# Kernel optimization log

Measured on AMD Instinct MI355X. Metric: run time of the kernel, lower is better.

Reference implementation:

```python
import jax, jax.numpy as jnp
import numpy as np
import math

IN_F, OUT_F, GRID = 1024, 1024, 7
BATCH, SEQ = 4, 4096


def _l2norm(v, eps=1e-12):
    return v / (jnp.linalg.norm(v) + eps)


def setup_inputs() -> dict:
    key = jax.random.key(0)
    k0, k1, k2, k3 = jax.random.split(key, 4)
    x = jax.random.normal(k0, (BATCH, SEQ, IN_F), dtype=jnp.float32)
    # spectral-normed base linear (weights nonzero for a meaningful baseline)
    base_w = jax.random.normal(k1, (OUT_F, IN_F), dtype=jnp.float32) * 0.02
    base_b = jnp.zeros((OUT_F,), dtype=jnp.float32)
    u = jax.random.normal(k2, (OUT_F,), dtype=jnp.float32)  # power-iteration buffer
    # Chebyshev translation points and fixed logspace scales (as in __init__)
    steps = jnp.arange(GRID, dtype=jnp.float32)
    translation = (-jnp.cos((2.0 * steps + 1.0) / (2.0 * GRID) * math.pi) * 1.5).reshape(1, 1, GRID)
    scale = (1.0 * jnp.logspace(-0.5, 0.5, GRID)).reshape(1, 1, GRID).astype(jnp.float32)
    wavelet_w = jax.random.normal(k3, (OUT_F, IN_F * GRID), dtype=jnp.float32) * 0.01
    soft_threshold = jnp.array([0.005], dtype=jnp.float32)
    output_scale = jnp.array([1.0], dtype=jnp.float32)
    return dict(x=x, base_w=base_w, base_b=base_b, u=u, translation=translation,
                scale=scale, wavelet_w=wavelet_w, soft_threshold=soft_threshold,
                output_scale=output_scale)


def reference(x, base_w, base_b, u, translation, scale, wavelet_w, soft_threshold, output_scale):
    x_flat = x.reshape(-1, x.shape[-1])  # [N, IN]
    # spectral norm: one power iteration (no grad through u, v), sigma = u' W v
    v = jax.lax.stop_gradient(_l2norm(base_w.T @ u))
    u2 = jax.lax.stop_gradient(_l2norm(base_w @ v))
    sigma = u2 @ (base_w @ v)
    w_sn = base_w / sigma
    base_out = jax.nn.silu(x_flat) @ w_sn.T + base_b  # [N, OUT]
    # wavelet (Ricker) basis expansion
    safe_scale = jnp.maximum(jnp.abs(scale), 0.1)  # [1,1,G]
    x_norm = jnp.tanh(x_flat) * 2.5  # [N, IN]
    xe = (x_norm[:, :, None] - translation) / safe_scale  # [N, IN, G]
    basis = (1.0 - xe * xe) * jnp.exp(-0.5 * xe * xe)
    kan = basis.reshape(x_flat.shape[0], -1) @ wavelet_w.T  # [N, OUT]
    thr = jax.nn.softplus(soft_threshold)
    kan = jnp.sign(kan) * jax.nn.relu(jnp.abs(kan) - thr)
    out = (base_out + kan) * output_scale
    return out.reshape(*x.shape[:-1], wavelet_w.shape[0])
```

## Files before the change

kernel.cpp:

```cpp
#include <hip/hip_runtime.h>
#include <math.h>


typedef __attribute__((ext_vector_type(4))) float  f32x4;
typedef __attribute__((ext_vector_type(8))) __bf16 bf16x8;
typedef __attribute__((ext_vector_type(8))) unsigned short u16x8;

#define NROWS 16384
#define INF   1024
#define OUTF  1024
#define GG    7
#define KKAN  7168
#define KTOT  8192

static __device__ __forceinline__ unsigned short f2bf(float f) {
  union { float f; unsigned int u; } v; v.f = f;
  unsigned int r = v.u + 0x7fffu + ((v.u >> 16) & 1u);
  return (unsigned short)(r >> 16);
}

__global__ void mv_wt_u(const float* __restrict__ W, const float* __restrict__ u,
                        float* __restrict__ t) {
  int j = blockIdx.x;
  int tid = threadIdx.x;
  float p = 0.f;
  for (int i = tid; i < OUTF; i += 256) p += W[(size_t)i * INF + j] * u[i];
  __shared__ float red[256];
  red[tid] = p; __syncthreads();
  for (int s = 128; s > 0; s >>= 1) { if (tid < s) red[tid] += red[tid + s]; __syncthreads(); }
  if (tid == 0) t[j] = red[0];
}

__global__ void mv_w_t(const float* __restrict__ W, const float* __restrict__ t,
                       float* __restrict__ s) {
  int i = blockIdx.x;
  int tid = threadIdx.x;
  float p = 0.f;
  for (int j = tid; j < INF; j += 256) p += W[(size_t)i * INF + j] * t[j];
  __shared__ float red[256];
  red[tid] = p; __syncthreads();
  for (int k = 128; k > 0; k >>= 1) { if (tid < k) red[tid] += red[tid + k]; __syncthreads(); }
  if (tid == 0) s[i] = red[0];
}

__global__ void sigma_finish(const float* __restrict__ t, const float* __restrict__ s,
                             const float* __restrict__ st, const float* __restrict__ os,
                             float* __restrict__ scal) {
  __shared__ float r1[256], r2[256];
  int tid = threadIdx.x;
  float p1 = 0.f, p2 = 0.f;
  for (int i = tid; i < 1024; i += 256) { float a = t[i]; p1 += a * a; float b = s[i]; p2 += b * b; }
  r1[tid] = p1; r2[tid] = p2; __syncthreads();
  for (int k = 128; k > 0; k >>= 1) { if (tid < k) { r1[tid] += r1[tid + k]; r2[tid] += r2[tid + k]; } __syncthreads(); }
  if (tid == 0) {
    float nt = sqrtf(r1[0]);
    float ns = sqrtf(r2[0]);
    float nq = ns / (nt + 1e-12f);
    float sigma = nq * nq / (nq + 1e-12f);
    scal[0] = 1.f / sigma;
    scal[1] = log1pf(__expf(st[0]));
    scal[2] = os[0];
  }
}

__global__ void wsn_cast(const float* __restrict__ w, const float* __restrict__ scal,
                         unsigned short* __restrict__ Wp) {
  float is = scal[0];
  int idx = blockIdx.x * 256 + threadIdx.x;
  int row = idx >> 7, i0 = (idx & 127) << 3;
  const f32x4* p = (const f32x4*)(w + (size_t)row * INF + i0);
  f32x4 a = p[0], b = p[1];
  u16x8 v;
  v[0] = f2bf(a[0] * is); v[1] = f2bf(a[1] * is); v[2] = f2bf(a[2] * is); v[3] = f2bf(a[3] * is);
  v[4] = f2bf(b[0] * is); v[5] = f2bf(b[1] * is); v[6] = f2bf(b[2] * is); v[7] = f2bf(b[3] * is);
  *(u16x8*)(Wp + (size_t)row * KTOT + KKAN + i0) = v;
}

__global__ void wkan_cast(const float* __restrict__ w, unsigned short* __restrict__ Wp) {
  __shared__ float row[KKAN];
  int orow = blockIdx.x;
  const float* src = w + (size_t)orow * KKAN;
  for (int c = threadIdx.x * 4; c < KKAN; c += 1024)
    *(f32x4*)&row[c] = *(const f32x4*)&src[c];
  __syncthreads();
  unsigned short* dst = Wp + (size_t)orow * KTOT;
  for (int r = threadIdx.x; r < 896; r += 256) {
    int g = r >> 7, i0 = (r & 127) << 3;
    u16x8 v;
#pragma unroll
    for (int j = 0; j < 8; j++) v[j] = f2bf(row[(i0 + j) * GG + g]);
    *(u16x8*)(dst + g * 1024 + i0) = v;
  }
}

__global__ void expand_kernel(const float* __restrict__ x,
                              const float* __restrict__ translation,
                              const float* __restrict__ scale,
                              unsigned short* __restrict__ Ap,
                              int row0, int nrows) {
  float tr[GG], iss[GG];
#pragma unroll
  for (int g = 0; g < GG; g++) {
    tr[g] = translation[g];
    float s = fabsf(scale[g]);
    iss[g] = 1.f / (s < 0.1f ? 0.1f : s);
  }
  int units = nrows * (INF / 8);
  int stride = gridDim.x * blockDim.x;
  for (int uu = blockIdx.x * blockDim.x + threadIdx.x; uu < units; uu += stride) {
    int nloc = uu >> 7;
    int i0 = (uu & 127) << 3;
    const f32x4* xp = (const f32x4*)(x + (size_t)(row0 + nloc) * INF + i0);
    f32x4 xa = xp[0], xb = xp[1];
    float xv[8] = {xa[0], xa[1], xa[2], xa[3], xb[0], xb[1], xb[2], xb[3]};
    u16x8 sb, kb[GG];
#pragma unroll
    for (int j = 0; j < 8; j++) {
      float xx = xv[j];
      float si = xx / (1.f + __expf(-xx));
      sb[j] = f2bf(si);
      float e2 = __expf(2.f * xx);
      float xn = 2.5f * (1.f - 2.f / (e2 + 1.f));
#pragma unroll
      for (int g = 0; g < GG; g++) {
        float xe = (xn - tr[g]) * iss[g];
        float t2 = xe * xe;
        float b = (1.f - t2) * __expf(-0.5f * t2);
        kb[g][j] = f2bf(b);
      }
    }
    unsigned short* rp = Ap + (size_t)nloc * KTOT;
    *(u16x8*)(rp + KKAN + i0) = sb;
#pragma unroll
    for (int g = 0; g < GG; g++) *(u16x8*)(rp + g * 1024 + i0) = kb[g];
  }
}

static __device__ __forceinline__ void gload16(const unsigned short* g, unsigned short* l) {
  __builtin_amdgcn_global_load_lds(
      (const __attribute__((address_space(1))) unsigned int*)g,
      (__attribute__((address_space(3))) unsigned int*)l, 16, 0, 0);
}

#define SCB   __builtin_amdgcn_sched_barrier(0)
#define SBAR  do { SCB; __builtin_amdgcn_s_barrier(); } while (0)
#define VM(N) asm volatile("s_waitcnt vmcnt(" #N ")" ::: "memory")
#define LG(N) asm volatile("s_waitcnt lgkmcnt(" #N ")" ::: "memory")

#define STAGE(db, tt) do { \
    const unsigned short* _sa = gA + (size_t)(tt) * 64; \
    const unsigned short* _sb = gB + (size_t)(tt) * 64; \
    unsigned short* _da = ldsS + (db) * 24576; \
    unsigned short* _db = ldsS + (db) * 24576 + 16384; \
    gload16(_sa,                       _da); \
    gload16(_sa + (size_t)64  * KTOT,  _da + 4096); \
    gload16(_sa + (size_t)128 * KTOT,  _da + 8192); \
    gload16(_sa + (size_t)192 * KTOT,  _da + 12288); \
    gload16(_sb,                       _db); \
    gload16(_sb + (size_t)64  * KTOT,  _db + 4096); \
  } while (0)

#define RD_A(dst, bb, kx) do { _Pragma("unroll") for (int i = 0; i < 4; ++i) \
    dst[i] = *(const bf16x8*)(pA + (bb) * 49152 + i * 2048 + (kx)); } while (0)

#define RD_B(dst, bb, kx) do { _Pragma("unroll") for (int j = 0; j < 4; ++j) \
    dst[j] = *(const bf16x8*)(pB + (bb) * 49152 + j * 2048 + (kx)); } while (0)

#define MM16(AF, BF) do { _Pragma("unroll") for (int i = 0; i < 4; ++i) \
    _Pragma("unroll") for (int j = 0; j < 4; ++j) \
      acc[i][j] = __builtin_amdgcn_mfma_f32_16x16x32_bf16(AF[i], BF[j], acc[i][j], 0, 0, 0); } while (0)

#define TILE(tt, bb, db, SS, WAIT) do { \
    RD_A(af0, bb, kx0); RD_B(bf0r, bb, kx0); \
    SCB; \
    RD_A(af1, bb, kx1); RD_B(bf1r, bb, kx1); \
    SCB; \
    if (SS) STAGE(db, (tt) + 2); \
    SCB; \
    LG(8); SCB; \
    __builtin_amdgcn_s_setprio(1); MM16(af0, bf0r); __builtin_amdgcn_s_setprio(0); \
    LG(0); SCB; \
    __builtin_amdgcn_s_setprio(1); MM16(af1, bf1r); __builtin_amdgcn_s_setprio(0); \
    WAIT; \
    SBAR; \
  } while (0)

__global__ __launch_bounds__(512, 2) void gemm_k(
    const unsigned short* __restrict__ A,
    const unsigned short* __restrict__ W,
    const float* __restrict__ bias,
    const float* __restrict__ scal,
    float* __restrict__ out) {
  __shared__ unsigned short lds[73728];

  int bid = blockIdx.x;
  int cpx = gridDim.x >> 3;
  int swz = (bid & 7) * cpx + (bid >> 3);
  int m0 = (swz >> 3) * 256;
  int n0 = (swz & 7) * 128;
  int tid = threadIdx.x;
  int wv = tid >> 6, l = tid & 63;
  int wr = wv >> 1, wc = wv & 1;

  float thr = scal[1], osc = scal[2];

  int rowq = tid >> 3;
  int swk = ((tid & 7) ^ (rowq & 7)) << 3;
  const unsigned short* gA = A + (size_t)(m0 + rowq) * KTOT + swk;
  const unsigned short* gB = W + (size_t)(n0 + rowq) * KTOT + swk;
  unsigned short* ldsS = lds + wv * 512;

  int lr = l & 15;
  int kx0 = (((l >> 4) << 4) ^ ((l & 7) << 4));
  int kx1 = kx0 ^ 64;
  const char* pA = (const char*)lds + (wr * 64 + lr) * 128;
  const char* pB = (const char*)lds + 32768 + (wc * 64 + lr) * 128;

  bf16x8 af0[4], af1[4], bf0r[4], bf1r[4];
  f32x4 acc[4][4] = {};

  STAGE(0, 0);
  STAGE(1, 1);
  VM(6);
  SBAR;

  for (int t = 0; t < 108; t += 3) {
    TILE(t,     0, 2, 1, VM(6));
    TILE(t + 1, 1, 0, 1, VM(6));
    TILE(t + 2, 2, 1, 1, VM(6));
  }
  TILE(108, 0, 2, 1, VM(6));
  TILE(109, 1, 0, 1, VM(6));
  TILE(110, 2, 1, 1, VM(6));
  TILE(111, 0, 2, 1, VM(6));

#pragma unroll
  for (int i = 0; i < 4; ++i)
#pragma unroll
    for (int j = 0; j < 4; ++j)
#pragma unroll
      for (int e = 0; e < 4; ++e) {
        float v = acc[i][j][e];
        float a = fabsf(v) - thr;
        a = a > 0.f ? a : 0.f;
        acc[i][j][e] = v > 0.f ? a : -a;
      }

  for (int t = 112; t < 124; t += 3) {
    TILE(t,     1, 0, 1, VM(6));
    TILE(t + 1, 2, 1, 1, VM(6));
    TILE(t + 2, 0, 2, 1, VM(6));
  }
  TILE(124, 1, 0, 1, VM(6));
  TILE(125, 2, 1, 1, VM(6));
  TILE(126, 0, 2, 0, VM(0));
  TILE(127, 1, 2, 0, (void)0);

  int rr = m0 + wr * 64 + ((l >> 4) << 2);
  int cc = n0 + wc * 64 + lr;
#pragma unroll
  for (int i = 0; i < 4; ++i)
#pragma unroll
    for (int j = 0; j < 4; ++j) {
      int c = cc + j * 16;
      float bc = bias[c];
#pragma unroll
      for (int e = 0; e < 4; ++e) {
        int r = rr + i * 16 + e;
        out[(size_t)r * OUTF + c] = (acc[i][j][e] + bc) * osc;
      }
    }
}

extern "C" void kernel_launch(void* const* d_in, const int* in_sizes, int n_in,
                              void* d_out, int out_size, void* d_ws, size_t ws_size,
                              hipStream_t stream) {
  const float* x              = (const float*)d_in[0];
  const float* base_w         = (const float*)d_in[1];
  const float* base_b         = (const float*)d_in[2];
  const float* u              = (const float*)d_in[3];
  const float* translation    = (const float*)d_in[4];
  const float* scale          = (const float*)d_in[5];
  const float* wavelet_w      = (const float*)d_in[6];
  const float* soft_threshold = (const float*)d_in[7];
  const float* output_scale   = (const float*)d_in[8];
  float* out = (float*)d_out;

  char* ws = (char*)d_ws;
  float* t_vec = (float*)ws;
  float* s_vec = t_vec + 1024;
  float* scal  = s_vec + 1024;
  unsigned short* Wp = (unsigned short*)(ws + 16384);
  char* dynbuf = ws + 16384 + (size_t)KTOT * OUTF * 2;

  size_t fixed = 16384 + (size_t)KTOT * OUTF * 2;
  size_t avail = ws_size > fixed ? ws_size - fixed : 0;

  mv_wt_u<<<1024, 256, 0, stream>>>(base_w, u, t_vec);
  mv_w_t<<<1024, 256, 0, stream>>>(base_w, t_vec, s_vec);
  sigma_finish<<<1, 256, 0, stream>>>(t_vec, s_vec, soft_threshold, output_scale, scal);
  wsn_cast<<<512, 256, 0, stream>>>(base_w, scal, Wp);
  wkan_cast<<<1024, 256, 0, stream>>>(wavelet_w, Wp);

  const size_t ROW = (size_t)KTOT * 2;
  size_t total = (size_t)NROWS * ROW;
  int nch = (int)((total + (avail > 0 ? avail : 1) - 1) / (avail > 0 ? avail : 1));
  if (nch < 1) nch = 1;
  long mc = (((NROWS + nch - 1) / nch) + 255) & ~255L;
  while (mc > 256 && (size_t)mc * ROW > avail) mc -= 256;
  if (mc < 256) mc = 256;

  unsigned short* Ap = (unsigned short*)dynbuf;

  for (long r0 = 0; r0 < NROWS; r0 += mc) {
    long nr = (NROWS - r0 < mc) ? (NROWS - r0) : mc;
    expand_kernel<<<2048, 256, 0, stream>>>(x, translation, scale, Ap, (int)r0, (int)nr);
    int mt = (int)(nr / 256);
    gemm_k<<<mt * 8, 512, 0, stream>>>(Ap, Wp, base_b, scal, out + (size_t)r0 * OUTF);
  }
}
```

Baseline: 333.6 us.

## Switch GEMM to 32x32x16 MFMA and coalesce the W^T u matvec

```diff
diff --git a/kernel.cpp b/kernel.cpp
--- a/kernel.cpp
+++ b/kernel.cpp
@@ -2,9 +2,10 @@
 #include <math.h>
 
 
-typedef __attribute__((ext_vector_type(4))) float  f32x4;
-typedef __attribute__((ext_vector_type(8))) __bf16 bf16x8;
-typedef __attribute__((ext_vector_type(8))) unsigned short u16x8;
+typedef __attribute__((ext_vector_type(4)))  float  f32x4;
+typedef __attribute__((ext_vector_type(16))) float  f32x16;
+typedef __attribute__((ext_vector_type(8)))  __bf16 bf16x8;
+typedef __attribute__((ext_vector_type(8)))  unsigned short u16x8;
 
 #define NROWS 16384
 #define INF   1024
@@ -19,16 +20,24 @@
   return (unsigned short)(r >> 16);
 }
 
-__global__ void mv_wt_u(const float* __restrict__ W, const float* __restrict__ u,
+__global__ void zero_t(float* __restrict__ t) { t[threadIdx.x] = 0.f; }
+
+__global__ void wtu_acc(const float* __restrict__ W, const float* __restrict__ u,
                         float* __restrict__ t) {
-  int j = blockIdx.x;
   int tid = threadIdx.x;
-  float p = 0.f;
-  for (int i = tid; i < OUTF; i += 256) p += W[(size_t)i * INF + j] * u[i];
-  __shared__ float red[256];
-  red[tid] = p; __syncthreads();
-  for (int s = 128; s > 0; s >>= 1) { if (tid < s) red[tid] += red[tid + s]; __syncthreads(); }
-  if (tid == 0) t[j] = red[0];
+  int j4 = tid * 4;
+  int i0 = blockIdx.x * 16;
+  f32x4 acc = {0.f, 0.f, 0.f, 0.f};
+  for (int i = i0; i < i0 + 16; ++i) {
+    float ui = u[i];
+    f32x4 w4 = *(const f32x4*)(W + (size_t)i * INF + j4);
+    acc[0] += w4[0] * ui; acc[1] += w4[1] * ui;
+    acc[2] += w4[2] * ui; acc[3] += w4[3] * ui;
+  }
+  atomicAdd(&t[j4 + 0], acc[0]);
+  atomicAdd(&t[j4 + 1], acc[1]);
+  atomicAdd(&t[j4 + 2], acc[2]);
+  atomicAdd(&t[j4 + 3], acc[3]);
 }
 
 __global__ void mv_w_t(const float* __restrict__ W, const float* __restrict__ t,
@@ -160,27 +169,31 @@
     gload16(_sb + (size_t)64  * KTOT,  _db + 4096); \
   } while (0)
 
-#define RD_A(dst, bb, kx) do { _Pragma("unroll") for (int i = 0; i < 4; ++i) \
-    dst[i] = *(const bf16x8*)(pA + (bb) * 49152 + i * 2048 + (kx)); } while (0)
-
-#define RD_B(dst, bb, kx) do { _Pragma("unroll") for (int j = 0; j < 4; ++j) \
-    dst[j] = *(const bf16x8*)(pB + (bb) * 49152 + j * 2048 + (kx)); } while (0)
-
-#define MM16(AF, BF) do { _Pragma("unroll") for (int i = 0; i < 4; ++i) \
-    _Pragma("unroll") for (int j = 0; j < 4; ++j) \
-      acc[i][j] = __builtin_amdgcn_mfma_f32_16x16x32_bf16(AF[i], BF[j], acc[i][j], 0, 0, 0); } while (0)
+#define RD4(dst, bb, kx) do { \
+    dst[0] = *(const bf16x8*)(pA + (bb) * 49152 + (kx)); \
+    dst[1] = *(const bf16x8*)(pA + (bb) * 49152 + 4096 + (kx)); \
+    dst[2] = *(const bf16x8*)(pB + (bb) * 49152 + (kx)); \
+    dst[3] = *(const bf16x8*)(pB + (bb) * 49152 + 4096 + (kx)); \
+  } while (0)
+
+#define MM4(F) do { \
+    acc[0][0] = __builtin_amdgcn_mfma_f32_32x32x16_bf16(F[0], F[2], acc[0][0], 0, 0, 0); \
+    acc[0][1] = __builtin_amdgcn_mfma_f32_32x32x16_bf16(F[0], F[3], acc[0][1], 0, 0, 0); \
+    acc[1][0] = __builtin_amdgcn_mfma_f32_32x32x16_bf16(F[1], F[2], acc[1][0], 0, 0, 0); \
+    acc[1][1] = __builtin_amdgcn_mfma_f32_32x32x16_bf16(F[1], F[3], acc[1][1], 0, 0, 0); \
+  } while (0)
 
 #define TILE(tt, bb, db, SS, WAIT) do { \
-    RD_A(af0, bb, kx0); RD_B(bf0r, bb, kx0); \
+    RD4(g0a, bb, kx0); RD4(g0b, bb, kx1); \
     SCB; \
-    RD_A(af1, bb, kx1); RD_B(bf1r, bb, kx1); \
+    RD4(g1a, bb, kx2); RD4(g1b, bb, kx3); \
     SCB; \
     if (SS) STAGE(db, (tt) + 2); \
     SCB; \
     LG(8); SCB; \
-    __builtin_amdgcn_s_setprio(1); MM16(af0, bf0r); __builtin_amdgcn_s_setprio(0); \
+    __builtin_amdgcn_s_setprio(1); MM4(g0a); MM4(g0b); __builtin_amdgcn_s_setprio(0); \
     LG(0); SCB; \
-    __builtin_amdgcn_s_setprio(1); MM16(af1, bf1r); __builtin_amdgcn_s_setprio(0); \
+    __builtin_amdgcn_s_setprio(1); MM4(g1a); MM4(g1b); __builtin_amdgcn_s_setprio(0); \
     WAIT; \
     SBAR; \
   } while (0)
@@ -210,14 +223,18 @@
   const unsigned short* gB = W + (size_t)(n0 + rowq) * KTOT + swk;
   unsigned short* ldsS = lds + wv * 512;
 
-  int lr = l & 15;
-  int kx0 = (((l >> 4) << 4) ^ ((l & 7) << 4));
-  int kx1 = kx0 ^ 64;
-  const char* pA = (const char*)lds + (wr * 64 + lr) * 128;
-  const char* pB = (const char*)lds + 32768 + (wc * 64 + lr) * 128;
-
-  bf16x8 af0[4], af1[4], bf0r[4], bf1r[4];
-  f32x4 acc[4][4] = {};
+  int l31 = l & 31;
+  int hi  = l >> 5;
+  int r7x = (l & 7) << 4;
+  int kx0 = (((0 * 2 + hi) << 4) ^ r7x);
+  int kx1 = (((1 * 2 + hi) << 4) ^ r7x);
+  int kx2 = (((2 * 2 + hi) << 4) ^ r7x);
+  int kx3 = (((3 * 2 + hi) << 4) ^ r7x);
+  const char* pA = (const char*)lds + (wr * 64 + l31) * 128;
+  const char* pB = (const char*)lds + 32768 + (wc * 64 + l31) * 128;
+
+  bf16x8 g0a[4], g0b[4], g1a[4], g1b[4];
+  f32x16 acc[2][2] = {};
 
   STAGE(0, 0);
   STAGE(1, 1);
@@ -235,11 +252,11 @@
   TILE(111, 0, 2, 1, VM(6));
 
 #pragma unroll
-  for (int i = 0; i < 4; ++i)
-#pragma unroll
-    for (int j = 0; j < 4; ++j)
-#pragma unroll
-      for (int e = 0; e < 4; ++e) {
+  for (int i = 0; i < 2; ++i)
+#pragma unroll
+    for (int j = 0; j < 2; ++j)
+#pragma unroll
+      for (int e = 0; e < 16; ++e) {
         float v = acc[i][j][e];
         float a = fabsf(v) - thr;
         a = a > 0.f ? a : 0.f;
@@ -256,17 +273,17 @@
   TILE(126, 0, 2, 0, VM(0));
   TILE(127, 1, 2, 0, (void)0);
 
-  int rr = m0 + wr * 64 + ((l >> 4) << 2);
-  int cc = n0 + wc * 64 + lr;
-#pragma unroll
-  for (int i = 0; i < 4; ++i)
-#pragma unroll
-    for (int j = 0; j < 4; ++j) {
-      int c = cc + j * 16;
+  int rr = m0 + wr * 64 + 4 * hi;
+  int cc = n0 + wc * 64 + l31;
+#pragma unroll
+  for (int i = 0; i < 2; ++i)
+#pragma unroll
+    for (int j = 0; j < 2; ++j) {
+      int c = cc + j * 32;
       float bc = bias[c];
 #pragma unroll
-      for (int e = 0; e < 4; ++e) {
-        int r = rr + i * 16 + e;
+      for (int e = 0; e < 16; ++e) {
+        int r = rr + i * 32 + (e & 3) + 8 * (e >> 2);
         out[(size_t)r * OUTF + c] = (acc[i][j][e] + bc) * osc;
       }
     }
@@ -296,7 +313,8 @@
   size_t fixed = 16384 + (size_t)KTOT * OUTF * 2;
   size_t avail = ws_size > fixed ? ws_size - fixed : 0;
 
-  mv_wt_u<<<1024, 256, 0, stream>>>(base_w, u, t_vec);
+  zero_t<<<1, 1024, 0, stream>>>(t_vec);
+  wtu_acc<<<64, 256, 0, stream>>>(base_w, u, t_vec);
   mv_w_t<<<1024, 256, 0, stream>>>(base_w, t_vec, s_vec);
   sigma_finish<<<1, 256, 0, stream>>>(t_vec, s_vec, soft_threshold, output_scale, scal);
   wsn_cast<<<512, 256, 0, stream>>>(base_w, scal, Wp);
```

After: 376.4 us. 12.8% more time.

## Software-pipeline LDS fragment reads across tiles and coalesce W^T u matvec

Applied to the files above, without the earlier changes.

```diff
diff --git a/kernel.cpp b/kernel.cpp
--- a/kernel.cpp
+++ b/kernel.cpp
@@ -19,16 +19,24 @@
   return (unsigned short)(r >> 16);
 }
 
-__global__ void mv_wt_u(const float* __restrict__ W, const float* __restrict__ u,
+__global__ void zero_t(float* __restrict__ t) { t[threadIdx.x] = 0.f; }
+
+__global__ void wtu_acc(const float* __restrict__ W, const float* __restrict__ u,
                         float* __restrict__ t) {
-  int j = blockIdx.x;
   int tid = threadIdx.x;
-  float p = 0.f;
-  for (int i = tid; i < OUTF; i += 256) p += W[(size_t)i * INF + j] * u[i];
-  __shared__ float red[256];
-  red[tid] = p; __syncthreads();
-  for (int s = 128; s > 0; s >>= 1) { if (tid < s) red[tid] += red[tid + s]; __syncthreads(); }
-  if (tid == 0) t[j] = red[0];
+  int j4 = tid * 4;
+  int i0 = blockIdx.x * 16;
+  f32x4 acc = {0.f, 0.f, 0.f, 0.f};
+  for (int i = i0; i < i0 + 16; ++i) {
+    float ui = u[i];
+    f32x4 w4 = *(const f32x4*)(W + (size_t)i * INF + j4);
+    acc[0] += w4[0] * ui; acc[1] += w4[1] * ui;
+    acc[2] += w4[2] * ui; acc[3] += w4[3] * ui;
+  }
+  atomicAdd(&t[j4 + 0], acc[0]);
+  atomicAdd(&t[j4 + 1], acc[1]);
+  atomicAdd(&t[j4 + 2], acc[2]);
+  atomicAdd(&t[j4 + 3], acc[3]);
 }
 
 __global__ void mv_w_t(const float* __restrict__ W, const float* __restrict__ t,
@@ -160,29 +168,29 @@
     gload16(_sb + (size_t)64  * KTOT,  _db + 4096); \
   } while (0)
 
-#define RD_A(dst, bb, kx) do { _Pragma("unroll") for (int i = 0; i < 4; ++i) \
-    dst[i] = *(const bf16x8*)(pA + (bb) * 49152 + i * 2048 + (kx)); } while (0)
-
-#define RD_B(dst, bb, kx) do { _Pragma("unroll") for (int j = 0; j < 4; ++j) \
-    dst[j] = *(const bf16x8*)(pB + (bb) * 49152 + j * 2048 + (kx)); } while (0)
-
-#define MM16(AF, BF) do { _Pragma("unroll") for (int i = 0; i < 4; ++i) \
+#define RD8(FA, FB, bb, kx) do { \
+    _Pragma("unroll") for (int i = 0; i < 4; ++i) \
+      FA[i] = *(const bf16x8*)(pA + (bb) * 49152 + i * 2048 + (kx)); \
     _Pragma("unroll") for (int j = 0; j < 4; ++j) \
-      acc[i][j] = __builtin_amdgcn_mfma_f32_16x16x32_bf16(AF[i], BF[j], acc[i][j], 0, 0, 0); } while (0)
-
-#define TILE(tt, bb, db, SS, WAIT) do { \
-    RD_A(af0, bb, kx0); RD_B(bf0r, bb, kx0); \
-    SCB; \
-    RD_A(af1, bb, kx1); RD_B(bf1r, bb, kx1); \
+      FB[j] = *(const bf16x8*)(pB + (bb) * 49152 + j * 2048 + (kx)); \
+  } while (0)
+
+#define MM16(FA, FB) do { _Pragma("unroll") for (int i = 0; i < 4; ++i) \
+    _Pragma("unroll") for (int j = 0; j < 4; ++j) \
+      acc[i][j] = __builtin_amdgcn_mfma_f32_16x16x32_bf16(FA[i], FB[j], acc[i][j], 0, 0, 0); } while (0)
+
+#define TILE(tt, bb, nb, db, SS, NR, W1) do { \
+    RD8(fYA, fYB, bb, kx1); \
     SCB; \
     if (SS) STAGE(db, (tt) + 2); \
     SCB; \
-    LG(8); SCB; \
-    __builtin_amdgcn_s_setprio(1); MM16(af0, bf0r); __builtin_amdgcn_s_setprio(0); \
+    __builtin_amdgcn_s_setprio(1); MM16(fXA, fXB); __builtin_amdgcn_s_setprio(0); \
     LG(0); SCB; \
-    __builtin_amdgcn_s_setprio(1); MM16(af1, bf1r); __builtin_amdgcn_s_setprio(0); \
-    WAIT; \
+    W1; \
     SBAR; \
+    if (NR) { RD8(fXA, fXB, nb, kx0); SCB; } \
+    __builtin_amdgcn_s_setprio(1); MM16(fYA, fYB); __builtin_amdgcn_s_setprio(0); \
+    LG(0); SCB; \
   } while (0)
 
 __global__ __launch_bounds__(512, 2) void gemm_k(
@@ -211,28 +219,32 @@
   unsigned short* ldsS = lds + wv * 512;
 
   int lr = l & 15;
-  int kx0 = (((l >> 4) << 4) ^ ((l & 7) << 4));
-  int kx1 = kx0 ^ 64;
+  int kb = (l >> 4) << 4;
+  int xr = (l & 7) << 4;
+  int kx0 = kb ^ xr;
+  int kx1 = (64 | kb) ^ xr;
   const char* pA = (const char*)lds + (wr * 64 + lr) * 128;
   const char* pB = (const char*)lds + 32768 + (wc * 64 + lr) * 128;
 
-  bf16x8 af0[4], af1[4], bf0r[4], bf1r[4];
+  bf16x8 fXA[4], fXB[4], fYA[4], fYB[4];
   f32x4 acc[4][4] = {};
 
   STAGE(0, 0);
   STAGE(1, 1);
   VM(6);
   SBAR;
+  RD8(fXA, fXB, 0, kx0);
+  LG(0); SCB;
 
   for (int t = 0; t < 108; t += 3) {
-    TILE(t,     0, 2, 1, VM(6));
-    TILE(t + 1, 1, 0, 1, VM(6));
-    TILE(t + 2, 2, 1, 1, VM(6));
-  }
-  TILE(108, 0, 2, 1, VM(6));
-  TILE(109, 1, 0, 1, VM(6));
-  TILE(110, 2, 1, 1, VM(6));
-  TILE(111, 0, 2, 1, VM(6));
+    TILE(t,     0, 1, 2, 1, 1, VM(6));
+    TILE(t + 1, 1, 2, 0, 1, 1, VM(6));
+    TILE(t + 2, 2, 0, 1, 1, 1, VM(6));
+  }
+  TILE(108, 0, 1, 2, 1, 1, VM(6));
+  TILE(109, 1, 2, 0, 1, 1, VM(6));
+  TILE(110, 2, 0, 1, 1, 1, VM(6));
+  TILE(111, 0, 1, 2, 1, 1, VM(6));
 
 #pragma unroll
   for (int i = 0; i < 4; ++i)
@@ -247,14 +259,14 @@
       }
 
   for (int t = 112; t < 124; t += 3) {
-    TILE(t,     1, 0, 1, VM(6));
-    TILE(t + 1, 2, 1, 1, VM(6));
-    TILE(t + 2, 0, 2, 1, VM(6));
-  }
-  TILE(124, 1, 0, 1, VM(6));
-  TILE(125, 2, 1, 1, VM(6));
-  TILE(126, 0, 2, 0, VM(0));
-  TILE(127, 1, 2, 0, (void)0);
+    TILE(t,     1, 2, 0, 1, 1, VM(6));
+    TILE(t + 1, 2, 0, 1, 1, 1, VM(6));
+    TILE(t + 2, 0, 1, 2, 1, 1, VM(6));
+  }
+  TILE(124, 1, 2, 0, 1, 1, VM(6));
+  TILE(125, 2, 0, 1, 1, 1, VM(6));
+  TILE(126, 0, 1, 2, 0, 1, VM(0));
+  TILE(127, 1, 2, 0, 0, 0, (void)0);
 
   int rr = m0 + wr * 64 + ((l >> 4) << 2);
   int cc = n0 + wc * 64 + lr;
@@ -296,7 +308,8 @@
   size_t fixed = 16384 + (size_t)KTOT * OUTF * 2;
   size_t avail = ws_size > fixed ? ws_size - fixed : 0;
 
-  mv_wt_u<<<1024, 256, 0, stream>>>(base_w, u, t_vec);
+  zero_t<<<1, 1024, 0, stream>>>(t_vec);
+  wtu_acc<<<64, 256, 0, stream>>>(base_w, u, t_vec);
   mv_w_t<<<1024, 256, 0, stream>>>(base_w, t_vec, s_vec);
   sigma_finish<<<1, 256, 0, stream>>>(t_vec, s_vec, soft_threshold, output_scale, scal);
   wsn_cast<<<512, 256, 0, stream>>>(base_w, scal, Wp);
```

Result: no change. 334.1 us (+0.2%).
